# Kernel optimization log

Hardware: AMD Instinct MI355X
Metric: run time of the kernel (lower is better)

The kernel has to match this reference:

```python
import jax, jax.numpy as jnp
import numpy as np

N, E, F_IN, H1, H2, C, G = 100000, 1600000, 128, 128, 64, 10, 64

def setup_inputs() -> dict:
    key = jax.random.key(0)
    ks = jax.random.split(key, 10)
    x = jax.random.normal(ks[0], (N, F_IN), dtype=jnp.float32)
    edge_index = jax.random.randint(ks[1], (2, E), 0, N, dtype=jnp.int32)
    batch = jnp.sort(jax.random.randint(ks[2], (N,), 0, G, dtype=jnp.int32))
    W1 = jax.random.normal(ks[3], (F_IN, H1), dtype=jnp.float32) * 0.05
    b1 = jnp.zeros((H1,), dtype=jnp.float32)
    W2 = jax.random.normal(ks[4], (H1, H2), dtype=jnp.float32) * 0.05
    b2 = jnp.zeros((H2,), dtype=jnp.float32)
    Wfc = jax.random.normal(ks[5], (H2, C), dtype=jnp.float32) * 0.05
    bfc = jnp.zeros((C,), dtype=jnp.float32)
    return {"x": x, "edge_index": edge_index, "batch": batch,
            "W1": W1, "b1": b1, "W2": W2, "b2": b2, "Wfc": Wfc, "bfc": bfc}

def gcn_conv(x, src, dst, W, b, n_nodes):
    # PyG GCNConv: add self-loops, symmetric normalization D^-1/2 A D^-1/2, linear, bias
    h = x @ W  # [N, H]
    deg = jnp.zeros((n_nodes,), h.dtype).at[dst].add(1.0) + 1.0  # +1 self-loop
    dinv = jax.lax.rsqrt(deg)
    norm = dinv[src] * dinv[dst]  # [E]
    msg = h[src] * norm[:, None]  # gather + scale
    agg = jnp.zeros_like(h).at[dst].add(msg)  # scatter-add at target
    agg = agg + h * (dinv * dinv)[:, None]    # self-loop messages
    return agg + b

def global_mean_pool(x, batch, num_graphs):
    sums = jnp.zeros((num_graphs, x.shape[1]), x.dtype).at[batch].add(x)
    cnt = jnp.zeros((num_graphs,), x.dtype).at[batch].add(1.0)
    return sums / jnp.maximum(cnt, 1.0)[:, None]

def reference(x, edge_index, batch, W1, b1, W2, b2, Wfc, bfc):
    src, dst = edge_index[0], edge_index[1]
    h = gcn_conv(x, src, dst, W1, b1, N)
    h = jax.nn.relu(h)
    # dropout is identity in eval mode
    h = gcn_conv(h, src, dst, W2, b2, N)
    g = global_mean_pool(h, batch, G)  # [G, 64]
    return g @ Wfc + bfc  # [G, C]
```

## Files before the change

### kernel.cpp

```cpp
#include <hip/hip_runtime.h>
#include <cstdint>

#define NN   100000
#define NE   1600000
#define FIN  128
#define HH1  128
#define HH2  64
#define NC   10
#define NG   64

#define NB   1024
#define NPB  98
#define BCAP 2048
#define EPB  8192
#define NBLK_B ((NE + EPB - 1) / EPB)

typedef __attribute__((ext_vector_type(8))) short bf16x8;
typedef __attribute__((ext_vector_type(4))) float f32x4;
typedef __attribute__((ext_vector_type(2))) float f32x2;

#if defined(__has_builtin)
#  if __has_builtin(__builtin_amdgcn_cvt_pk_f32_fp8) && \
      __has_builtin(__builtin_amdgcn_cvt_f32_fp8) && \
      __has_builtin(__builtin_amdgcn_cvt_pk_fp8_f32)
#    define HW_FP8 1
#  endif
#endif
#ifndef HW_FP8
#  define HW_FP8 0
#endif

__device__ __forceinline__ unsigned pack2(float a, float b) {
    union { float f; unsigned u; } x, y; x.f = a; y.f = b;
    const unsigned lo = x.u + 0x7fffu + ((x.u >> 16) & 1u);
    const unsigned hi = y.u + 0x7fffu + ((y.u >> 16) & 1u);
    return (lo >> 16) | (hi & 0xffff0000u);
}

__device__ __forceinline__ float sw_dec8(unsigned b) {
    const unsigned s = b >> 7, e = (b >> 3) & 15u, m = b & 7u;
    float v;
    if (e == 0) v = (float)m * 0.001953125f;
    else { union { unsigned u; float f; } y; y.u = ((e + 120u) << 23) | (m << 20); v = y.f; }
    return s ? -v : v;
}
__device__ __forceinline__ unsigned sw_enc8(float f) {
    union { float f; unsigned u; } x; x.f = f;
    const unsigned s = (x.u >> 31) << 7;
    float a = fabsf(f);
    a = fminf(a, 448.0f);
    unsigned ia;
    if (a < 0.015625f) {
        ia = (unsigned)(int)rintf(a * 512.0f);
    } else {
        union { float f; unsigned u; } y; y.f = a;
        int e = (int)((y.u >> 23) & 255u) - 127;
        unsigned keep = (y.u >> 20) & 7u;
        const unsigned rest = y.u & 0xfffffu;
        keep += (rest > 0x80000u) || (rest == 0x80000u && (keep & 1u));
        if (keep == 8u) { keep = 0u; e += 1; }
        if (e >= 8) { e = 8; if (keep > 6u) keep = 6u; }
        ia = ((unsigned)(e + 7) << 3) | keep;
    }
    return s | ia;
}
__device__ __forceinline__ f32x4 fp8x4_f32(unsigned u) {
#if HW_FP8
    f32x2 lo = __builtin_amdgcn_cvt_pk_f32_fp8(u, false);
    f32x2 hi = __builtin_amdgcn_cvt_pk_f32_fp8(u, true);
    return (f32x4){lo[0], lo[1], hi[0], hi[1]};
#else
    return (f32x4){sw_dec8(u & 0xffu), sw_dec8((u >> 8) & 0xffu),
                   sw_dec8((u >> 16) & 0xffu), sw_dec8(u >> 24)};
#endif
}
__device__ __forceinline__ float fp8_f32(unsigned b) {
#if HW_FP8
    return __builtin_amdgcn_cvt_f32_fp8(b, 0);
#else
    return sw_dec8(b & 0xffu);
#endif
}
__device__ __forceinline__ unsigned f32_fp8(float a) {
#if HW_FP8
    return __builtin_amdgcn_cvt_pk_fp8_f32(a, a, 0u, false) & 0xffu;
#else
    return sw_enc8(a);
#endif
}
__device__ __forceinline__ unsigned pack4_fp8(float a, float b, float c, float d) {
#if HW_FP8
    unsigned u = __builtin_amdgcn_cvt_pk_fp8_f32(a, b, 0u, false);
    u = __builtin_amdgcn_cvt_pk_fp8_f32(c, d, u, true);
    return u;
#else
    return sw_enc8(a) | (sw_enc8(b) << 8) | (sw_enc8(c) << 16) | (sw_enc8(d) << 24);
#endif
}

__global__ __launch_bounds__(256) void k_init(int* __restrict__ gcursor,
                                              float* __restrict__ sums) {
    const int i = blockIdx.x * blockDim.x + threadIdx.x;
    if (i < NB) gcursor[i] = i * BCAP;
    if (i < NG * HH2 + NG) sums[i] = 0.f;
}

__global__ __launch_bounds__(256) void k_bscatter(const int* __restrict__ src,
                                                  const int* __restrict__ dst,
                                                  int* __restrict__ gcursor,
                                                  unsigned* __restrict__ pairs, int E) {
    __shared__ int cnt[NB];
    __shared__ int cur[NB];
    const int t = threadIdx.x;
    for (int j = t; j < NB; j += 256) cnt[j] = 0;
    __syncthreads();
    const int base = blockIdx.x * EPB;
#pragma unroll
    for (int i = 0; i < EPB / 1024; ++i) {
        const int e = base + i * 1024 + t * 4;
        if (e < E) {
            const int4 d = *(const int4*)&dst[e];
            atomicAdd(&cnt[(unsigned)d.x / NPB], 1);
            atomicAdd(&cnt[(unsigned)d.y / NPB], 1);
            atomicAdd(&cnt[(unsigned)d.z / NPB], 1);
            atomicAdd(&cnt[(unsigned)d.w / NPB], 1);
        }
    }
    __syncthreads();
    for (int j = t; j < NB; j += 256) {
        const int c = cnt[j];
        if (c) cur[j] = atomicAdd(&gcursor[j], c);
    }
    __syncthreads();
#pragma unroll
    for (int i = 0; i < EPB / 1024; ++i) {
        const int e = base + i * 1024 + t * 4;
        if (e < E) {
            const int4 d = *(const int4*)&dst[e];
            const int4 s = *(const int4*)&src[e];
            int p; unsigned bk, lo;
            bk = (unsigned)d.x / NPB; lo = d.x - bk * NPB;
            p = atomicAdd(&cur[bk], 1); pairs[p] = ((unsigned)s.x << 7) | lo;
            bk = (unsigned)d.y / NPB; lo = d.y - bk * NPB;
            p = atomicAdd(&cur[bk], 1); pairs[p] = ((unsigned)s.y << 7) | lo;
            bk = (unsigned)d.z / NPB; lo = d.z - bk * NPB;
            p = atomicAdd(&cur[bk], 1); pairs[p] = ((unsigned)s.z << 7) | lo;
            bk = (unsigned)d.w / NPB; lo = d.w - bk * NPB;
            p = atomicAdd(&cur[bk], 1); pairs[p] = ((unsigned)s.w << 7) | lo;
        }
    }
}

__global__ __launch_bounds__(256) void k_csr(const unsigned* __restrict__ pairs,
                                             const int* __restrict__ gcursor,
                                             int* __restrict__ row_start,
                                             int* __restrict__ rend,
                                             float* __restrict__ dinv,
                                             int* __restrict__ esrc) {
    const int b = blockIdx.x;
    const int node0 = b * NPB;
    if (node0 >= NN) return;
    const int nn = min(NPB, NN - node0);
    __shared__ int cnt[NPB];
    __shared__ int scn[128];
    __shared__ int cur[NPB];
    const int t = threadIdx.x;
    if (t < NPB) cnt[t] = 0;
    __syncthreads();
    const int ebeg = b * BCAP, eend = gcursor[b];
    for (int j = ebeg + t; j < eend; j += 256)
        atomicAdd(&cnt[pairs[j] & 127u], 1);
    __syncthreads();
    int v = 0, pv = 0;
    if (t < 128) { v = (t < nn) ? cnt[t] : 0; pv = (v + 3) & ~3; scn[t] = pv; }
    __syncthreads();
    for (int off = 1; off < 128; off <<= 1) {
        int x = 0;
        if (t < 128 && t >= off) x = scn[t - off];
        __syncthreads();
        if (t < 128) scn[t] += x;
        __syncthreads();
    }
    if (t < nn) {
        const int rs = ebeg + scn[t] - pv;
        row_start[node0 + t] = rs;
        rend[node0 + t]      = rs + v;
        cur[t] = rs;
        dinv[node0 + t] = rsqrtf((float)v + 1.f);
    }
    __syncthreads();
    for (int j = ebeg + t; j < eend; j += 256) {
        const unsigned p = pairs[j];
        const int pos = atomicAdd(&cur[p & 127u], 1);
        esrc[pos] = (int)(p >> 7);
    }
}

template <int BN, bool ABF16>
__global__ __launch_bounds__(256) void k_mfma(const void* __restrict__ Ain,
                                              const float* __restrict__ Bin,
                                              unsigned char* __restrict__ Cout,
                                              const float* __restrict__ rowscale,
                                              int M) {
    __shared__ unsigned short Bs[BN][128];
    const int t = threadIdx.x;
    const int row0 = blockIdx.x * 128;

    {
        constexpr int KSEG = (BN == 128) ? 64 : 32;
        const int n  = t & (BN - 1);
        const int kb = (t / BN) * KSEG;
#pragma unroll
        for (int i = 0; i < KSEG; i += 2) {
            const int k = kb + i;
            const unsigned u = pack2(Bin[(size_t)k * BN + n], Bin[(size_t)(k + 1) * BN + n]);
            *(unsigned*)&Bs[n][(((k >> 3) ^ (n & 7)) << 3) + (k & 7)] = u;
        }
    }

    const int lane = t & 63, wave = t >> 6;
    const int lr = lane & 15, lg = lane >> 4;
    constexpr int MR = 2;
    constexpr int NR = BN / 16;
    const int wrow = wave * 32;

    bf16x8 afrag[4][MR];
#pragma unroll
    for (int m = 0; m < MR; ++m) {
        int row = row0 + wrow + m * 16 + lr;
        row = (row < M) ? row : (M - 1);
        if (ABF16) {
            const uint4* ap = (const uint4*)((const unsigned short*)Ain + (size_t)row * 128);
#pragma unroll
            for (int ks = 0; ks < 4; ++ks) {
                const uint4 v = ap[ks * 4 + lg];
                afrag[ks][m] = *(const bf16x8*)&v;
            }
        } else {
            const float* ap = (const float*)Ain + (size_t)row * 128;
#pragma unroll
            for (int ks = 0; ks < 4; ++ks) {
                const float4 f0 = *(const float4*)(ap + ks * 32 + lg * 8);
                const float4 f1 = *(const float4*)(ap + ks * 32 + lg * 8 + 4);
                const uint4 v = make_uint4(pack2(f0.x, f0.y), pack2(f0.z, f0.w),
                                           pack2(f1.x, f1.y), pack2(f1.z, f1.w));
                afrag[ks][m] = *(const bf16x8*)&v;
            }
        }
    }
    __syncthreads();

    f32x4 acc[MR][NR];
#pragma unroll
    for (int m = 0; m < MR; ++m)
#pragma unroll
        for (int n = 0; n < NR; ++n) acc[m][n] = (f32x4){0.f, 0.f, 0.f, 0.f};

#pragma unroll
    for (int ks = 0; ks < 4; ++ks) {
        const int cc = ((ks * 4 + lg) ^ (lr & 7)) * 8;
        bf16x8 b[NR];
#pragma unroll
        for (int n = 0; n < NR; ++n) b[n] = *(const bf16x8*)&Bs[n * 16 + lr][cc];
#pragma unroll
        for (int m = 0; m < MR; ++m)
#pragma unroll
            for (int n = 0; n < NR; ++n)
                acc[m][n] = __builtin_amdgcn_mfma_f32_16x16x32_bf16(afrag[ks][m], b[n], acc[m][n], 0, 0, 0);
    }

#pragma unroll
    for (int m = 0; m < MR; ++m) {
        const int rb = wrow + m * 16 + lg * 4;
        float s[4]; int gr[4];
#pragma unroll
        for (int j = 0; j < 4; ++j) {
            gr[j] = row0 + rb + j;
            s[j] = (gr[j] < M) ? rowscale[gr[j]] : 0.f;
        }
#pragma unroll
        for (int n = 0; n < NR; ++n) {
            const int col = n * 16 + lr;
#pragma unroll
            for (int j = 0; j < 4; ++j)
                if (gr[j] < M)
                    Cout[(size_t)gr[j] * BN + col] = (unsigned char)f32_fp8(acc[m][n][j] * s[j]);
        }
    }
}

__global__ __launch_bounds__(256) void k_agg1(const int* __restrict__ row_start,
                                              const int* __restrict__ row_end,
                                              const int* __restrict__ esrc,
                                              const float* __restrict__ dinv,
                                              const uint2* __restrict__ hb,
                                              const float* __restrict__ b,
                                              uint4* __restrict__ outp, int n) {
    const int wid  = (blockIdx.x * blockDim.x + threadIdx.x) >> 6;
    const int lane = threadIdx.x & 63;
    if (wid >= n) return;
    const int q  = lane >> 4;
    const int ql = lane & 15;
    const int beg = row_start[wid], end = row_end[wid];

    f32x4 accA = (f32x4){0.f, 0.f, 0.f, 0.f};
    f32x4 accB = accA;
    if (q == 0) {
        const uint2 u = hb[(size_t)wid * 16 + ql];
        accA = fp8x4_f32(u.x);
        accB = fp8x4_f32(u.y);
    }

    int j = beg;
    for (; j + 16 <= end; j += 16) {
        const int4 ix = *(const int4*)&esrc[j + q * 4];
        const uint2 u0 = hb[(size_t)ix.x * 16 + ql];
        const uint2 u1 = hb[(size_t)ix.y * 16 + ql];
        const uint2 u2 = hb[(size_t)ix.z * 16 + ql];
        const uint2 u3 = hb[(size_t)ix.w * 16 + ql];
        accA += (fp8x4_f32(u0.x) + fp8x4_f32(u1.x)) + (fp8x4_f32(u2.x) + fp8x4_f32(u3.x));
        accB += (fp8x4_f32(u0.y) + fp8x4_f32(u1.y)) + (fp8x4_f32(u2.y) + fp8x4_f32(u3.y));
    }
    for (; j + 4 <= end; j += 4) {
        const uint2 u = hb[(size_t)esrc[j + q] * 16 + ql];
        accA += fp8x4_f32(u.x);
        accB += fp8x4_f32(u.y);
    }
    if (j + q < end) {
        const uint2 u = hb[(size_t)esrc[j + q] * 16 + ql];
        accA += fp8x4_f32(u.x);
        accB += fp8x4_f32(u.y);
    }

#pragma unroll
    for (int k = 0; k < 4; ++k) {
        accA[k] += __shfl_xor(accA[k], 16); accA[k] += __shfl_xor(accA[k], 32);
        accB[k] += __shfl_xor(accB[k], 16); accB[k] += __shfl_xor(accB[k], 32);
    }

    if (q == 0) {
        const float dd = dinv[wid];
        const float4 bv0 = *(const float4*)&b[ql * 8];
        const float4 bv1 = *(const float4*)&b[ql * 8 + 4];
        float r[8];
        r[0] = fmaxf(fmaf(dd, accA[0], bv0.x), 0.f);
        r[1] = fmaxf(fmaf(dd, accA[1], bv0.y), 0.f);
        r[2] = fmaxf(fmaf(dd, accA[2], bv0.z), 0.f);
        r[3] = fmaxf(fmaf(dd, accA[3], bv0.w), 0.f);
        r[4] = fmaxf(fmaf(dd, accB[0], bv1.x), 0.f);
        r[5] = fmaxf(fmaf(dd, accB[1], bv1.y), 0.f);
        r[6] = fmaxf(fmaf(dd, accB[2], bv1.z), 0.f);
        r[7] = fmaxf(fmaf(dd, accB[3], bv1.w), 0.f);
        outp[(size_t)wid * 16 + ql] = make_uint4(pack2(r[0], r[1]), pack2(r[2], r[3]),
                                                 pack2(r[4], r[5]), pack2(r[6], r[7]));
    }
}

__global__ __launch_bounds__(256) void k_agg2(const int* __restrict__ row_start,
                                              const int* __restrict__ row_end,
                                              const int* __restrict__ esrc,
                                              const float* __restrict__ dinv,
                                              const uint2* __restrict__ hb,
                                              const float* __restrict__ b,
                                              uint2* __restrict__ outp, int n) {
    const int wid  = (blockIdx.x * blockDim.x + threadIdx.x) >> 6;
    const int lane = threadIdx.x & 63;
    if (wid >= n) return;
    const int o  = lane >> 3;
    const int ol = lane & 7;
    const int beg = row_start[wid], end = row_end[wid];

    f32x4 accA = (f32x4){0.f, 0.f, 0.f, 0.f};
    f32x4 accB = accA;
    if (o == 0) {
        const uint2 u = hb[(size_t)wid * 8 + ol];
        accA = fp8x4_f32(u.x);
        accB = fp8x4_f32(u.y);
    }

    int j = beg;
    for (; j + 16 <= end; j += 16) {
        const int2 ix = *(const int2*)&esrc[j + o * 2];
        const uint2 u0 = hb[(size_t)ix.x * 8 + ol];
        const uint2 u1 = hb[(size_t)ix.y * 8 + ol];
        accA += fp8x4_f32(u0.x) + fp8x4_f32(u1.x);
        accB += fp8x4_f32(u0.y) + fp8x4_f32(u1.y);
    }
    for (; j + 8 <= end; j += 8) {
        const uint2 u = hb[(size_t)esrc[j + o] * 8 + ol];
        accA += fp8x4_f32(u.x);
        accB += fp8x4_f32(u.y);
    }
    if (j + o < end) {
        const uint2 u = hb[(size_t)esrc[j + o] * 8 + ol];
        accA += fp8x4_f32(u.x);
        accB += fp8x4_f32(u.y);
    }

#pragma unroll
    for (int k = 0; k < 4; ++k) {
        accA[k] += __shfl_xor(accA[k], 8);
        accA[k] += __shfl_xor(accA[k], 16);
        accA[k] += __shfl_xor(accA[k], 32);
        accB[k] += __shfl_xor(accB[k], 8);
        accB[k] += __shfl_xor(accB[k], 16);
        accB[k] += __shfl_xor(accB[k], 32);
    }

    if (o == 0) {
        const float dd = dinv[wid];
        const float4 bv0 = *(const float4*)&b[ol * 8];
        const float4 bv1 = *(const float4*)&b[ol * 8 + 4];
        const unsigned w0 = pack4_fp8(fmaf(dd, accA[0], bv0.x), fmaf(dd, accA[1], bv0.y),
                                      fmaf(dd, accA[2], bv0.z), fmaf(dd, accA[3], bv0.w));
        const unsigned w1 = pack4_fp8(fmaf(dd, accB[0], bv1.x), fmaf(dd, accB[1], bv1.y),
                                      fmaf(dd, accB[2], bv1.z), fmaf(dd, accB[3], bv1.w));
        outp[(size_t)wid * 8 + ol] = make_uint2(w0, w1);
    }
}

__global__ __launch_bounds__(256) void k_pool(const unsigned char* __restrict__ v2,
                                              const int* __restrict__ batch,
                                              float* __restrict__ sums,
                                              float* __restrict__ cnt, int n) {
    constexpr int NPW = 128;
    const int gt = blockIdx.x * blockDim.x + threadIdx.x;
    const int wave = gt >> 6;
    const int lane = threadIdx.x & 63;
    const int start = wave * NPW;
    if (start >= n) return;
    const int end = min(start + NPW, n);
    float acc = 0.f, cacc = 0.f;
    int cur = batch[start];
    for (int nd = start; nd < end; ++nd) {
        const int gid = batch[nd];
        if (gid != cur) {
            atomicAdd(&sums[cur * HH2 + lane], acc);
            if (lane == 0) atomicAdd(&cnt[cur], cacc);
            acc = 0.f; cacc = 0.f; cur = gid;
        }
        acc += fp8_f32(v2[(size_t)nd * 64 + lane]);
        cacc += 1.f;
    }
    atomicAdd(&sums[cur * HH2 + lane], acc);
    if (lane == 0) atomicAdd(&cnt[cur], cacc);
}

__global__ void k_fc(const float* __restrict__ sums, const float* __restrict__ cnt,
                     const float* __restrict__ Wfc, const float* __restrict__ bfc,
                     float* __restrict__ out) {
    const int tid = threadIdx.x;
    if (tid >= NG * NC) return;
    const int g = tid / NC;
    const int c = tid % NC;
    float a = 0.f;
    for (int k = 0; k < HH2; ++k)
        a = fmaf(sums[g * HH2 + k], Wfc[k * NC + c], a);
    const float cg = fmaxf(cnt[g], 1.0f);
    out[g * NC + c] = a / cg + bfc[c];
}

extern "C" void kernel_launch(void* const* d_in, const int* in_sizes, int n_in,
                              void* d_out, int out_size, void* d_ws, size_t ws_size,
                              hipStream_t stream) {
    const float* x   = (const float*)d_in[0];
    const int*   ei  = (const int*)d_in[1];
    const int*   bat = (const int*)d_in[2];
    const float* W1  = (const float*)d_in[3];
    const float* b1  = (const float*)d_in[4];
    const float* W2  = (const float*)d_in[5];
    const float* b2  = (const float*)d_in[6];
    const float* Wfc = (const float*)d_in[7];
    const float* bfc = (const float*)d_in[8];
    float* out = (float*)d_out;

    const int* src = ei;
    const int* dst = ei + NE;

    float* ws = (float*)d_ws;
    unsigned* relu1     = (unsigned*)ws;
    unsigned char* v2   = (unsigned char*)ws;
    unsigned char* h1b  = (unsigned char*)(ws + (size_t)NN * 64);
    unsigned char* h2b  = (unsigned char*)(ws + (size_t)NN * 64);
    float*    dinv      = ws + (size_t)NN * 96;
    int*      row_start = (int*)(ws + (size_t)NN * 97);
    int*      rend      = (int*)(ws + (size_t)NN * 98);
    int*      esrc      = (int*)(ws + (size_t)NN * 99);
    unsigned* pairs     = (unsigned*)(ws + (size_t)NN * 99 + (size_t)NB * BCAP);
    float*    sums      = ws + (size_t)NN * 99 + 2 * (size_t)NB * BCAP;
    float*    cntf      = sums + NG * HH2;
    int*      gcursor   = (int*)(cntf + NG);

    k_init<<<(NG * HH2 + NG + 255) / 256, 256, 0, stream>>>(gcursor, sums);
    k_bscatter<<<NBLK_B, 256, 0, stream>>>(src, dst, gcursor, pairs, NE);
    k_csr<<<NB, 256, 0, stream>>>(pairs, gcursor, row_start, rend, dinv, esrc);

    const int gblk = (NN + 127) / 128;

    k_mfma<128, false><<<gblk, 256, 0, stream>>>(x, W1, h1b, dinv, NN);
    k_agg1<<<(NN * 64 + 255) / 256, 256, 0, stream>>>(row_start, rend, esrc, dinv,
                                                      (const uint2*)h1b, b1,
                                                      (uint4*)relu1, NN);

    k_mfma<64, true><<<gblk, 256, 0, stream>>>(relu1, W2, h2b, dinv, NN);
    k_agg2<<<(NN * 64 + 255) / 256, 256, 0, stream>>>(row_start, rend, esrc, dinv,
                                                      (const uint2*)h2b, b2,
                                                      (uint2*)v2, NN);

    {
        const int waves = (NN + 127) / 128;
        const int blocks = (waves * 64 + 255) / 256;
        k_pool<<<blocks, 256, 0, stream>>>(v2, bat, sums, cntf, NN);
    }

    k_fc<<<1, 640, 0, stream>>>(sums, cntf, Wfc, bfc, out);
}
```

Before: 224.4 us.

## Replace single-pass 1024-bucket edge scatter with two-level 32x32 radix split

The one-pass binning of edges into 1024 destination buckets becomes a two-level radix partition: first into 32 coarse buckets, then each coarse bucket into 32 fine buckets of 98 nodes. Each pass uses only 32 shared counters and writes to 32 output streams, which should give more coalesced scattered writes and fewer global cursor atomics. The cost is an extra kernel launch and one more read and write of the full edge list through a new intermediate buffer, and coarse buckets can overflow if the degree distribution is skewed.

```diff
diff --git a/kernel.cpp b/kernel.cpp
--- a/kernel.cpp
+++ b/kernel.cpp
@@ -12,8 +12,12 @@
 #define NB   1024
 #define NPB  98
 #define BCAP 2048
-#define EPB  8192
-#define NBLK_B ((NE + EPB - 1) / EPB)
+#define NCB  32
+#define NPCB 3136
+#define CCAP 53248
+#define EPS  2048
+#define NBLK1 ((NE + EPS - 1) / EPS)
+#define SLICES (CCAP / EPS)
 
 typedef __attribute__((ext_vector_type(8))) short bf16x8;
 typedef __attribute__((ext_vector_type(4))) float f32x4;
@@ -98,61 +102,89 @@
 #endif
 }
 
-__global__ __launch_bounds__(256) void k_init(int* __restrict__ gcursor,
+__global__ __launch_bounds__(256) void k_init(int* __restrict__ gcur1,
+                                              int* __restrict__ gcur2,
                                               float* __restrict__ sums) {
     const int i = blockIdx.x * blockDim.x + threadIdx.x;
-    if (i < NB) gcursor[i] = i * BCAP;
+    if (i < NCB) gcur1[i] = i * CCAP;
+    if (i < NB)  gcur2[i] = i * BCAP;
     if (i < NG * HH2 + NG) sums[i] = 0.f;
 }
 
-__global__ __launch_bounds__(256) void k_bscatter(const int* __restrict__ src,
-                                                  const int* __restrict__ dst,
-                                                  int* __restrict__ gcursor,
-                                                  unsigned* __restrict__ pairs, int E) {
-    __shared__ int cnt[NB];
-    __shared__ int cur[NB];
+__global__ __launch_bounds__(256) void k_split1(const int* __restrict__ src,
+                                                const int* __restrict__ dst,
+                                                int* __restrict__ gcur1,
+                                                unsigned* __restrict__ pairs1, int E) {
+    __shared__ int bcnt[NCB];
+    __shared__ int bglob[NCB];
     const int t = threadIdx.x;
-    for (int j = t; j < NB; j += 256) cnt[j] = 0;
-    __syncthreads();
-    const int base = blockIdx.x * EPB;
-#pragma unroll
-    for (int i = 0; i < EPB / 1024; ++i) {
-        const int e = base + i * 1024 + t * 4;
+    if (t < NCB) bcnt[t] = 0;
+    __syncthreads();
+    const int base = blockIdx.x * EPS;
+    unsigned val[8]; int bo[8];
+#pragma unroll
+    for (int i = 0; i < 8; ++i) {
+        const int e = base + i * 256 + t;
         if (e < E) {
-            const int4 d = *(const int4*)&dst[e];
-            atomicAdd(&cnt[(unsigned)d.x / NPB], 1);
-            atomicAdd(&cnt[(unsigned)d.y / NPB], 1);
-            atomicAdd(&cnt[(unsigned)d.z / NPB], 1);
-            atomicAdd(&cnt[(unsigned)d.w / NPB], 1);
-        }
-    }
-    __syncthreads();
-    for (int j = t; j < NB; j += 256) {
-        const int c = cnt[j];
-        if (c) cur[j] = atomicAdd(&gcursor[j], c);
-    }
-    __syncthreads();
-#pragma unroll
-    for (int i = 0; i < EPB / 1024; ++i) {
-        const int e = base + i * 1024 + t * 4;
-        if (e < E) {
-            const int4 d = *(const int4*)&dst[e];
-            const int4 s = *(const int4*)&src[e];
-            int p; unsigned bk, lo;
-            bk = (unsigned)d.x / NPB; lo = d.x - bk * NPB;
-            p = atomicAdd(&cur[bk], 1); pairs[p] = ((unsigned)s.x << 7) | lo;
-            bk = (unsigned)d.y / NPB; lo = d.y - bk * NPB;
-            p = atomicAdd(&cur[bk], 1); pairs[p] = ((unsigned)s.y << 7) | lo;
-            bk = (unsigned)d.z / NPB; lo = d.z - bk * NPB;
-            p = atomicAdd(&cur[bk], 1); pairs[p] = ((unsigned)s.z << 7) | lo;
-            bk = (unsigned)d.w / NPB; lo = d.w - bk * NPB;
-            p = atomicAdd(&cur[bk], 1); pairs[p] = ((unsigned)s.w << 7) | lo;
+            const int d = dst[e], s = src[e];
+            const int c = d / NPCB;
+            val[i] = ((unsigned)s << 12) | (unsigned)(d - c * NPCB);
+            const int l = atomicAdd(&bcnt[c], 1);
+            bo[i] = (c << 16) | l;
+        } else bo[i] = -1;
+    }
+    __syncthreads();
+    if (t < NCB && bcnt[t] > 0) bglob[t] = atomicAdd(&gcur1[t], bcnt[t]);
+    __syncthreads();
+#pragma unroll
+    for (int i = 0; i < 8; ++i) {
+        if (bo[i] >= 0) {
+            const int c = bo[i] >> 16, l = bo[i] & 0xffff;
+            pairs1[bglob[c] + l] = val[i];
+        }
+    }
+}
+
+__global__ __launch_bounds__(256) void k_split2(const unsigned* __restrict__ pairs1,
+                                                const int* __restrict__ gcur1,
+                                                int* __restrict__ gcur2,
+                                                unsigned* __restrict__ pairs2) {
+    __shared__ int bcnt[NCB];
+    __shared__ int bglob[NCB];
+    const int t = threadIdx.x;
+    const int c = blockIdx.x / SLICES;
+    const int sidx = blockIdx.x % SLICES;
+    const int start = c * CCAP + sidx * EPS;
+    const int cend = gcur1[c];
+    if (t < NCB) bcnt[t] = 0;
+    __syncthreads();
+    unsigned val[8]; int bo[8];
+#pragma unroll
+    for (int i = 0; i < 8; ++i) {
+        const int e = start + i * 256 + t;
+        if (e < cend) {
+            const unsigned p = pairs1[e];
+            const unsigned r = p & 4095u;
+            const int f = (int)r / NPB;
+            val[i] = ((p >> 12) << 7) | (r - (unsigned)(f * NPB));
+            const int l = atomicAdd(&bcnt[f], 1);
+            bo[i] = (f << 16) | l;
+        } else bo[i] = -1;
+    }
+    __syncthreads();
+    if (t < NCB && bcnt[t] > 0) bglob[t] = atomicAdd(&gcur2[c * NCB + t], bcnt[t]);
+    __syncthreads();
+#pragma unroll
+    for (int i = 0; i < 8; ++i) {
+        if (bo[i] >= 0) {
+            const int f = bo[i] >> 16, l = bo[i] & 0xffff;
+            pairs2[bglob[f] + l] = val[i];
         }
     }
 }
 
 __global__ __launch_bounds__(256) void k_csr(const unsigned* __restrict__ pairs,
-                                             const int* __restrict__ gcursor,
+                                             const int* __restrict__ gcur2,
                                              int* __restrict__ row_start,
                                              int* __restrict__ rend,
                                              float* __restrict__ dinv,
@@ -167,7 +199,7 @@
     const int t = threadIdx.x;
     if (t < NPB) cnt[t] = 0;
     __syncthreads();
-    const int ebeg = b * BCAP, eend = gcursor[b];
+    const int ebeg = b * BCAP, eend = gcur2[b];
     for (int j = ebeg + t; j < eend; j += 256)
         atomicAdd(&cnt[pairs[j] & 127u], 1);
     __syncthreads();
@@ -486,14 +518,17 @@
     int*      row_start = (int*)(ws + (size_t)NN * 97);
     int*      rend      = (int*)(ws + (size_t)NN * 98);
     int*      esrc      = (int*)(ws + (size_t)NN * 99);
-    unsigned* pairs     = (unsigned*)(ws + (size_t)NN * 99 + (size_t)NB * BCAP);
-    float*    sums      = ws + (size_t)NN * 99 + 2 * (size_t)NB * BCAP;
+    unsigned* pairs2    = (unsigned*)(ws + (size_t)NN * 99 + (size_t)NB * BCAP);
+    unsigned* pairs1    = (unsigned*)(ws + (size_t)NN * 99 + 2 * (size_t)NB * BCAP);
+    float*    sums      = ws + (size_t)NN * 99 + 2 * (size_t)NB * BCAP + (size_t)NCB * CCAP;
     float*    cntf      = sums + NG * HH2;
-    int*      gcursor   = (int*)(cntf + NG);
-
-    k_init<<<(NG * HH2 + NG + 255) / 256, 256, 0, stream>>>(gcursor, sums);
-    k_bscatter<<<NBLK_B, 256, 0, stream>>>(src, dst, gcursor, pairs, NE);
-    k_csr<<<NB, 256, 0, stream>>>(pairs, gcursor, row_start, rend, dinv, esrc);
+    int*      gcur1     = (int*)(cntf + NG);
+    int*      gcur2     = gcur1 + NCB;
+
+    k_init<<<(NG * HH2 + NG + 255) / 256, 256, 0, stream>>>(gcur1, gcur2, sums);
+    k_split1<<<NBLK1, 256, 0, stream>>>(src, dst, gcur1, pairs1, NE);
+    k_split2<<<NCB * SLICES, 256, 0, stream>>>(pairs1, gcur1, gcur2, pairs2);
+    k_csr<<<NB, 256, 0, stream>>>(pairs2, gcur2, row_start, rend, dinv, esrc);
 
     const int gblk = (NN + 127) / 128;
 
```

Measured after the change: 231.9 us. 3.3% more time.
